# Optimization experiments

Measured on AMD Instinct MI355X. Metric: run time of the kernel, lower is better.

Reference implementation:

```python
import jax, jax.numpy as jnp
import numpy as np
from jax import lax

P = 2048
HIDDEN = 512
NUM_STEPS = 15
BATCH = 8192
SLOPE = 25.0  # snntorch surrogate.fast_sigmoid default slope


@jax.custom_vjp
def spike_fn(x):
    # Heaviside forward, fast-sigmoid surrogate backward.
    return (x > 0).astype(x.dtype)

def _spike_fwd(x):
    return spike_fn(x), x

def _spike_bwd(x, g):
    return (g / (SLOPE * jnp.abs(x) + 1.0) ** 2,)

spike_fn.defvjp(_spike_fwd, _spike_bwd)


def setup_inputs() -> dict:
    key = jax.random.key(0)
    ks = jax.random.split(key, 6)
    x = jax.random.randint(ks[0], (BATCH, 2), 0, P)
    embed = jax.random.normal(ks[1], (P, HIDDEN), dtype=jnp.float32)
    # Linear weights stored [in, out] (transpose of torch convention, same math)
    W1 = jax.random.normal(ks[2], (2 * HIDDEN, HIDDEN), dtype=jnp.float32) * (1.0 / np.sqrt(2 * HIDDEN))
    b1 = jnp.zeros((HIDDEN,), dtype=jnp.float32)
    W2 = jax.random.normal(ks[3], (HIDDEN, P), dtype=jnp.float32) * (1.0 / np.sqrt(HIDDEN))
    b2 = jnp.zeros((P,), dtype=jnp.float32)
    beta1 = jnp.float32(0.9)
    thr1 = jnp.float32(1.0)
    beta2 = jnp.float32(0.9)
    thr2 = jnp.float32(1.0)
    return {"x": x, "embed": embed, "W1": W1, "b1": b1, "W2": W2, "b2": b2,
            "beta1": beta1, "thr1": thr1, "beta2": beta2, "thr2": thr2}


def reference(x, embed, W1, b1, W2, b2, beta1, thr1, beta2, thr2):
    # clamp params as in the torch no-grad block (identity at init values)
    beta1 = jnp.clip(beta1, 0.1, 0.9)
    beta2 = jnp.clip(beta2, 0.1, 0.9)
    thr1 = jnp.clip(thr1, 0.1, None)
    thr2 = jnp.clip(thr2, 0.1, None)

    emb = embed[x].reshape(x.shape[0], -1)          # [B, 2*hidden]
    cur1 = emb @ W1 + b1                            # constant across steps

    mem1_0 = jnp.zeros((x.shape[0], HIDDEN), dtype=jnp.float32)
    mem2_0 = jnp.zeros((x.shape[0], P), dtype=jnp.float32)

    def step(carry, _):
        mem1, mem2 = carry
        # snntorch Leaky, reset_mechanism='subtract': reset from PREVIOUS mem, detached
        reset1 = lax.stop_gradient((mem1 - thr1 > 0).astype(mem1.dtype))
        mem1 = beta1 * mem1 + cur1 - reset1 * thr1
        spk1 = spike_fn(mem1 - thr1)
        cur2 = spk1 @ W2 + b2
        # lif2 has reset_mechanism='none'
        mem2 = beta2 * mem2 + cur2
        return (mem1, mem2), None

    (mem1, mem2), _ = lax.scan(step, (mem1_0, mem2_0), None, length=NUM_STEPS)
    return mem2  # output = last mem2
```

## Files before the change

### kernel.cpp

```cpp
#include <hip/hip_runtime.h>
#include <hip/hip_bf16.h>
#include <stdint.h>

typedef float    f32x4 __attribute__((ext_vector_type(4)));
typedef _Float16 f16x4 __attribute__((ext_vector_type(4)));
typedef _Float16 f16x8 __attribute__((ext_vector_type(8)));

#define NSTEPS 15

__global__ __launch_bounds__(256) void prep_kernel(
    const float* __restrict__ embed, const float* __restrict__ W1,
    const float* __restrict__ W2, const float* __restrict__ b2,
    const float* __restrict__ beta2p,
    _Float16* __restrict__ Ap, _Float16* __restrict__ Btp,
    _Float16* __restrict__ W2T, float* __restrict__ bias2s)
{
  __shared__ _Float16 sh[2][64][72];
  const int b = blockIdx.x;
  const int t = threadIdx.x;

  if (b < 1024) {
    const int i  = b * 256 + t;
    const int m  = i >> 7;
    const int k4 = (i & 127) * 4;
    f32x4 v = *(const f32x4*)&embed[(size_t)m * 512 + k4];
    f16x4 h0, h1;
#pragma unroll
    for (int j = 0; j < 4; ++j) {
      h0[j] = (_Float16)v[j];
      h1[j] = (_Float16)(v[j] - (float)h0[j]);
    }
    _Float16* r = Ap + (size_t)m * 1024 + k4;
    *(f16x4*)(r)       = h0;
    *(f16x4*)(r + 512) = h1;
  } else if (b < 1152) {
    const int idx = b - 1024;
    const int n0 = (idx & 7) * 64;
    const int k0 = ((idx >> 3) & 7) * 64;
    const int z  = idx >> 6;
    const int kk = t >> 4;
    const int n4 = (t & 15) * 4;
#pragma unroll
    for (int i = 0; i < 4; ++i) {
      f32x4 v = *(const f32x4*)&W1[(size_t)(z * 512 + k0 + kk + i * 16) * 512 + n0 + n4];
#pragma unroll
      for (int j = 0; j < 4; ++j) {
        float s = v[j] * 64.0f;
        _Float16 hi = (_Float16)s;
        sh[0][n4 + j][kk + i * 16] = hi;
        sh[1][n4 + j][kk + i * 16] = (_Float16)(s - (float)hi);
      }
    }
    __syncthreads();
#pragma unroll
    for (int i = 0; i < 2; ++i) {
      const int nn = (t >> 3) + i * 32;
      const int k8 = (t & 7) * 8;
      _Float16* r = Btp + (size_t)(z * 512 + n0 + nn) * 1024 + k0 + k8;
      *(uint4*)(r)       = *(const uint4*)&sh[0][nn][k8];
      *(uint4*)(r + 512) = *(const uint4*)&sh[1][nn][k8];
    }
  } else if (b < 1408) {
    const int idx = b - 1152;
    const int n0 = (idx & 31) * 64;
    const int k0 = (idx >> 5) * 64;
    const int kk = t >> 4;
    const int n4 = (t & 15) * 4;
#pragma unroll
    for (int i = 0; i < 4; ++i) {
      f32x4 v = *(const f32x4*)&W2[(size_t)(k0 + kk + i * 16) * 2048 + n0 + n4];
#pragma unroll
      for (int j = 0; j < 4; ++j) sh[0][n4 + j][kk + i * 16] = (_Float16)v[j];
    }
    __syncthreads();
#pragma unroll
    for (int i = 0; i < 2; ++i) {
      const int nn = (t >> 3) + i * 32;
      const int k8 = (t & 7) * 8;
      *(uint4*)&W2T[(size_t)(n0 + nn) * 512 + k0 + k8] = *(const uint4*)&sh[0][nn][k8];
    }
  } else {
    const float beta2 = fminf(fmaxf(beta2p[0], 0.1f), 0.9f);
    float cb = 0.0f;
    for (int i = 0; i < NSTEPS; ++i) cb = beta2 * cb + 1.0f;
    const int n = (b - 1408) * 256 + t;
    if (n < 2048) bias2s[n] = cb * b2[n];
  }
}

__device__ __forceinline__ void gld_lds16(const void* g, void* l) {
  __builtin_amdgcn_global_load_lds(
      (const __attribute__((address_space(1))) uint32_t*)g,
      (__attribute__((address_space(3))) uint32_t*)l, 16, 0, 0);
}

__global__ __launch_bounds__(256) void gemm1_kernel(
    const _Float16* __restrict__ Ap,
    const _Float16* __restrict__ Btp,
    float* __restrict__ Tp)
{
  __shared__ __align__(16) char lds[(128 + 64) * 128];
  char* AsB = lds;
  char* BsB = lds + 128 * 128;

  const int t    = threadIdx.x;
  const int lane = t & 63;
  const int wave = t >> 6;
  const int z    = blockIdx.y;

  int bid = blockIdx.x;
  bid = (bid & 7) * 32 + (bid >> 3);
  const int m0 = (bid >> 4) * 128;
  const int n0 = (bid & 15) * 64;

  f32x4 acc[2][4] = {};

  for (int kt = 0; kt < 12; ++kt) {
    const int k0   = z * 768 + kt * 64;
    const int acol = (k0 < 1024) ? k0 : k0 - 1024;
    const int bcol = (k0 < 1024) ? (k0 & 511) : k0 - 512;
#pragma unroll
    for (int i = 0; i < 4; ++i) {
      const int ob  = i * 4096 + wave * 1024;
      const int o   = ob + lane * 16;
      const int row = o >> 7;
      const int c   = ((o >> 4) & 7) ^ (row & 7);
      gld_lds16(Ap + ((size_t)(m0 + row) * 1024 + acol + c * 8), AsB + ob);
    }
#pragma unroll
    for (int i = 0; i < 2; ++i) {
      const int ob  = i * 4096 + wave * 1024;
      const int o   = ob + lane * 16;
      const int row = o >> 7;
      const int c   = ((o >> 4) & 7) ^ (row & 7);
      gld_lds16(Btp + ((size_t)(n0 + row) * 1024 + bcol + c * 8), BsB + ob);
    }
    asm volatile("s_waitcnt vmcnt(0)" ::: "memory");
    __syncthreads();

#pragma unroll
    for (int kk = 0; kk < 2; ++kk) {
      const int lc = (lane >> 4) + kk * 4;
      f16x8 af[2], bf[4];
#pragma unroll
      for (int mi = 0; mi < 2; ++mi) {
        const int row = wave * 32 + mi * 16 + (lane & 15);
        af[mi] = *(const f16x8*)(AsB + row * 128 + ((lc ^ (row & 7)) << 4));
      }
#pragma unroll
      for (int ni = 0; ni < 4; ++ni) {
        const int row = ni * 16 + (lane & 15);
        bf[ni] = *(const f16x8*)(BsB + row * 128 + ((lc ^ (row & 7)) << 4));
      }
#pragma unroll
      for (int mi = 0; mi < 2; ++mi)
#pragma unroll
        for (int ni = 0; ni < 4; ++ni)
          acc[mi][ni] = __builtin_amdgcn_mfma_f32_16x16x32_f16(
              af[mi], bf[ni], acc[mi][ni], 0, 0, 0);
    }
    __syncthreads();
  }

  float* Cz = Tp + (size_t)z * 2048 * 1024;
#pragma unroll
  for (int mi = 0; mi < 2; ++mi) {
    const int r0 = m0 + wave * 32 + mi * 16 + ((lane >> 4) << 2);
#pragma unroll
    for (int ni = 0; ni < 4; ++ni) {
      const int cc = n0 + ni * 16 + (lane & 15);
#pragma unroll
      for (int q = 0; q < 4; ++q)
        Cz[(size_t)(r0 + q) * 1024 + cc] = acc[mi][ni][q] * 0.015625f;
    }
  }
}

__global__ __launch_bounds__(256) void recur_kernel(
    const int* __restrict__ x,
    const float* __restrict__ Tp,
    const float* __restrict__ b1,
    const float* __restrict__ beta1p, const float* __restrict__ thr1p,
    const float* __restrict__ beta2p,
    _Float16* __restrict__ S)
{
  const float beta1 = fminf(fmaxf(beta1p[0], 0.1f), 0.9f);
  const float thr1  = fmaxf(thr1p[0], 0.1f);
  const float beta2 = fminf(fmaxf(beta2p[0], 0.1f), 0.9f);
  const size_t ZS = (size_t)2048 * 1024;

  const int t = threadIdx.x;
  const int b = blockIdx.x * 4 + (t >> 6);
  const int h = (t & 63) * 8;
  const int x0 = x[b * 2 + 0];
  const int x1 = x[b * 2 + 1];

  const float* p00 = &Tp[(size_t)x0 * 1024 + h];
  const float* p01 = &Tp[(size_t)x1 * 1024 + 512 + h];

  float cur[8];
#pragma unroll
  for (int half = 0; half < 2; ++half) {
    f32x4 a0 = *(const f32x4*)(p00 + half * 4);
    f32x4 a1 = *(const f32x4*)(p00 + ZS + half * 4);
    f32x4 c0 = *(const f32x4*)(p01 + half * 4);
    f32x4 c1 = *(const f32x4*)(p01 + ZS + half * 4);
    f32x4 e  = *(const f32x4*)&b1[h + half * 4];
#pragma unroll
    for (int j = 0; j < 4; ++j)
      cur[half * 4 + j] = (a0[j] + a1[j]) + (c0[j] + c1[j]) + e[j];
  }

  float m[8] = {}, s[8] = {};
#pragma unroll
  for (int st = 0; st < NSTEPS; ++st) {
#pragma unroll
    for (int j = 0; j < 8; ++j) {
      float r = (m[j] > thr1) ? thr1 : 0.0f;
      m[j] = beta1 * m[j] + cur[j] - r;
      float sp = (m[j] > thr1) ? 1.0f : 0.0f;
      s[j] = beta2 * s[j] + sp;
    }
  }

  __align__(16) _Float16 o[8];
#pragma unroll
  for (int j = 0; j < 8; ++j) o[j] = (_Float16)s[j];
  *(uint4*)&S[(size_t)b * 512 + h] = *(const uint4*)o;
}

__device__ __forceinline__ void g2_round(
    const _Float16* __restrict__ A, const _Float16* __restrict__ Bt,
    char* lds, int m0, int n0, int wave, int lane, int tile, int r)
{
  const int k0 = tile * 64;
  char* lb = lds + (tile % 3) * 49152;
  if (r < 4) {
    const int ob  = r * 8192 + wave * 1024;
    const int o   = ob + lane * 16;
    const int row = o >> 7;
    const int c   = ((o >> 4) & 7) ^ (row & 7);
    gld_lds16(A + ((size_t)(m0 + row) * 512 + k0 + c * 8), lb + ob);
  } else {
    const int ob  = (r - 4) * 8192 + wave * 1024;
    const int o   = ob + lane * 16;
    const int row = o >> 7;
    const int c   = ((o >> 4) & 7) ^ (row & 7);
    gld_lds16(Bt + ((size_t)(n0 + row) * 512 + k0 + c * 8), lb + 32768 + ob);
  }
}

template<int QA>
__device__ __forceinline__ void g2_mfma16(
    f32x4 (&acc)[8][2], const f16x8 (&af)[4][2], const f16x8 (&bf)[2][2])
{
#pragma unroll
  for (int kk = 0; kk < 2; ++kk)
#pragma unroll
    for (int mi = 0; mi < 4; ++mi)
#pragma unroll
      for (int ni = 0; ni < 2; ++ni)
        acc[QA * 4 + mi][ni] = __builtin_amdgcn_mfma_f32_16x16x32_f16(
            af[mi][kk], bf[ni][kk], acc[QA * 4 + mi][ni], 0, 0, 0);
}

template<int QA>
__device__ __forceinline__ void g2_lda(
    f16x8 (&af)[4][2], const char* lb, int wm, int lane)
{
#pragma unroll
  for (int mi = 0; mi < 4; ++mi) {
    const int row = wm * 128 + QA * 64 + mi * 16 + (lane & 15);
#pragma unroll
    for (int kk = 0; kk < 2; ++kk) {
      const int lc = (lane >> 4) + kk * 4;
      af[mi][kk] = *(const f16x8*)(lb + row * 128 + ((lc ^ (row & 7)) << 4));
    }
  }
}

__device__ __forceinline__ void g2_ldb(
    f16x8 (&bf)[2][2], const char* lb, int wn, int lane)
{
#pragma unroll
  for (int ni = 0; ni < 2; ++ni) {
    const int row = wn * 32 + ni * 16 + (lane & 15);
#pragma unroll
    for (int kk = 0; kk < 2; ++kk) {
      const int lc = (lane >> 4) + kk * 4;
      bf[ni][kk] = *(const f16x8*)(lb + 32768 + row * 128 + ((lc ^ (row & 7)) << 4));
    }
  }
}

__global__ __launch_bounds__(512, 2) void gemm2_pipe_kernel(
    const _Float16* __restrict__ A,
    const _Float16* __restrict__ Bt,
    const float* __restrict__ bias,
    float* __restrict__ C)
{
  __shared__ __align__(16) char lds[3 * 49152];

  const int t    = threadIdx.x;
  const int lane = t & 63;
  const int wave = t >> 6;
  const int wm   = wave >> 2;
  const int wn   = wave & 3;

  int bid = blockIdx.x;
  bid = (bid & 7) * 64 + (bid >> 3);
  const int m0 = (bid >> 4) * 256;
  const int n0 = (bid & 15) * 128;

  f32x4 acc[8][2] = {};
  f16x8 af[4][2], bf[2][2];

#pragma unroll
  for (int r = 0; r < 6; ++r) g2_round(A, Bt, lds, m0, n0, wave, lane, 0, r);
#pragma unroll
  for (int r = 0; r < 6; ++r) g2_round(A, Bt, lds, m0, n0, wave, lane, 1, r);
  asm volatile("s_waitcnt vmcnt(6)" ::: "memory");
  __builtin_amdgcn_s_barrier();

  for (int tt = 0; tt < 8; ++tt) {
    const char* lb = lds + (tt % 3) * 49152;
    const bool pf = (tt + 2 < 8);

    g2_lda<0>(af, lb, wm, lane);
    g2_ldb(bf, lb, wn, lane);
    if (pf) {
      g2_round(A, Bt, lds, m0, n0, wave, lane, tt + 2, 0);
      g2_round(A, Bt, lds, m0, n0, wave, lane, tt + 2, 1);
      g2_round(A, Bt, lds, m0, n0, wave, lane, tt + 2, 2);
    }
    __builtin_amdgcn_s_barrier();
    asm volatile("s_waitcnt lgkmcnt(0)" ::: "memory");
    __builtin_amdgcn_s_setprio(1);
    g2_mfma16<0>(acc, af, bf);
    __builtin_amdgcn_s_setprio(0);
    __builtin_amdgcn_s_barrier();

    g2_lda<1>(af, lb, wm, lane);
    if (pf) {
      g2_round(A, Bt, lds, m0, n0, wave, lane, tt + 2, 3);
      g2_round(A, Bt, lds, m0, n0, wave, lane, tt + 2, 4);
      g2_round(A, Bt, lds, m0, n0, wave, lane, tt + 2, 5);
    }
    __builtin_amdgcn_s_barrier();
    asm volatile("s_waitcnt lgkmcnt(0)" ::: "memory");
    __builtin_amdgcn_s_setprio(1);
    g2_mfma16<1>(acc, af, bf);
    __builtin_amdgcn_s_setprio(0);
    asm volatile("s_waitcnt vmcnt(6)" ::: "memory");
    __builtin_amdgcn_s_barrier();
  }

#pragma unroll
  for (int a = 0; a < 8; ++a) {
    const int r0 = m0 + wm * 128 + a * 16 + ((lane >> 4) << 2);
#pragma unroll
    for (int ni = 0; ni < 2; ++ni) {
      const int cc = n0 + wn * 32 + ni * 16 + (lane & 15);
      const float bv = bias[cc];
#pragma unroll
      for (int q = 0; q < 4; ++q)
        C[(size_t)(r0 + q) * 2048 + cc] = acc[a][ni][q] + bv;
    }
  }
}

extern "C" void kernel_launch(void* const* d_in, const int* in_sizes, int n_in,
                              void* d_out, int out_size, void* d_ws, size_t ws_size,
                              hipStream_t stream) {
  const int*   x     = (const int*)  d_in[0];
  const float* embed = (const float*)d_in[1];
  const float* W1    = (const float*)d_in[2];
  const float* b1    = (const float*)d_in[3];
  const float* W2    = (const float*)d_in[4];
  const float* b2    = (const float*)d_in[5];
  const float* beta1 = (const float*)d_in[6];
  const float* thr1  = (const float*)d_in[7];
  const float* beta2 = (const float*)d_in[8];
  float* out = (float*)d_out;

  char* ws = (char*)d_ws;
  float*    Tp     = (float*)   ws;
  _Float16* Ap     = (_Float16*)(ws + (16u << 20));
  _Float16* Btp    = (_Float16*)(ws + (20u << 20));
  _Float16* W2T    = (_Float16*)(ws + (22u << 20));
  _Float16* S      = (_Float16*)(ws + (24u << 20));
  float*    bias2s = (float*)   (ws + (32u << 20));

  prep_kernel<<<dim3(1416), 256, 0, stream>>>(embed, W1, W2, b2, beta2,
                                              Ap, Btp, W2T, bias2s);

  gemm1_kernel<<<dim3(256, 2), 256, 0, stream>>>(Ap, Btp, Tp);

  recur_kernel<<<dim3(2048), 256, 0, stream>>>(x, Tp, b1, beta1, thr1, beta2, S);

  gemm2_pipe_kernel<<<dim3(512), 512, 0, stream>>>(S, W2T, bias2s, out);
}
```

Measured before the change: 65.23 us.

## Replace split-K gemm1 partial outputs with in-block K reduction and 32x32 MFMA

```diff
diff --git a/kernel.cpp b/kernel.cpp
--- a/kernel.cpp
+++ b/kernel.cpp
@@ -2,18 +2,18 @@
 #include <hip/hip_bf16.h>
 #include <stdint.h>
 
-typedef float    f32x4 __attribute__((ext_vector_type(4)));
-typedef _Float16 f16x4 __attribute__((ext_vector_type(4)));
-typedef _Float16 f16x8 __attribute__((ext_vector_type(8)));
+typedef float    f32x4  __attribute__((ext_vector_type(4)));
+typedef float    f32x16 __attribute__((ext_vector_type(16)));
+typedef _Float16 f16x4  __attribute__((ext_vector_type(4)));
+typedef _Float16 f16x8  __attribute__((ext_vector_type(8)));
 
 #define NSTEPS 15
 
 __global__ __launch_bounds__(256) void prep_kernel(
     const float* __restrict__ embed, const float* __restrict__ W1,
-    const float* __restrict__ W2, const float* __restrict__ b2,
-    const float* __restrict__ beta2p,
+    const float* __restrict__ W2,
     _Float16* __restrict__ Ap, _Float16* __restrict__ Btp,
-    _Float16* __restrict__ W2T, float* __restrict__ bias2s)
+    _Float16* __restrict__ W2T)
 {
   __shared__ _Float16 sh[2][64][72];
   const int b = blockIdx.x;
@@ -60,7 +60,7 @@
       *(uint4*)(r)       = *(const uint4*)&sh[0][nn][k8];
       *(uint4*)(r + 512) = *(const uint4*)&sh[1][nn][k8];
     }
-  } else if (b < 1408) {
+  } else {
     const int idx = b - 1152;
     const int n0 = (idx & 31) * 64;
     const int k0 = (idx >> 5) * 64;
@@ -79,12 +79,6 @@
       const int k8 = (t & 7) * 8;
       *(uint4*)&W2T[(size_t)(n0 + nn) * 512 + k0 + k8] = *(const uint4*)&sh[0][nn][k8];
     }
-  } else {
-    const float beta2 = fminf(fmaxf(beta2p[0], 0.1f), 0.9f);
-    float cb = 0.0f;
-    for (int i = 0; i < NSTEPS; ++i) cb = beta2 * cb + 1.0f;
-    const int n = (b - 1408) * 256 + t;
-    if (n < 2048) bias2s[n] = cb * b2[n];
   }
 }
 
@@ -94,91 +88,111 @@
       (__attribute__((address_space(3))) uint32_t*)l, 16, 0, 0);
 }
 
-__global__ __launch_bounds__(256) void gemm1_kernel(
+__global__ __launch_bounds__(512) void gemm1_kernel(
     const _Float16* __restrict__ Ap,
     const _Float16* __restrict__ Btp,
-    float* __restrict__ Tp)
-{
-  __shared__ __align__(16) char lds[(128 + 64) * 128];
-  char* AsB = lds;
-  char* BsB = lds + 128 * 128;
+    float* __restrict__ T)
+{
+  __shared__ __align__(16) char lds[49152];
+  char* const ALDS = lds;
+  char* const BLDS = lds + 32768;
 
   const int t    = threadIdx.x;
   const int lane = t & 63;
   const int wave = t >> 6;
-  const int z    = blockIdx.y;
+  const int kh   = wave >> 2;
+  const int wq   = wave & 3;
+  const int wm   = wq >> 1;
+  const int wn   = wq & 1;
 
   int bid = blockIdx.x;
   bid = (bid & 7) * 32 + (bid >> 3);
   const int m0 = (bid >> 4) * 128;
   const int n0 = (bid & 15) * 64;
 
-  f32x4 acc[2][4] = {};
+  f32x16 acc[2] = {};
 
   for (int kt = 0; kt < 12; ++kt) {
-    const int k0   = z * 768 + kt * 64;
-    const int acol = (k0 < 1024) ? k0 : k0 - 1024;
-    const int bcol = (k0 < 1024) ? (k0 & 511) : k0 - 512;
-#pragma unroll
-    for (int i = 0; i < 4; ++i) {
-      const int ob  = i * 4096 + wave * 1024;
-      const int o   = ob + lane * 16;
-      const int row = o >> 7;
-      const int c   = ((o >> 4) & 7) ^ (row & 7);
-      gld_lds16(Ap + ((size_t)(m0 + row) * 1024 + acol + c * 8), AsB + ob);
-    }
-#pragma unroll
-    for (int i = 0; i < 2; ++i) {
-      const int ob  = i * 4096 + wave * 1024;
-      const int o   = ob + lane * 16;
-      const int row = o >> 7;
-      const int c   = ((o >> 4) & 7) ^ (row & 7);
-      gld_lds16(Btp + ((size_t)(n0 + row) * 1024 + bcol + c * 8), BsB + ob);
+#pragma unroll
+    for (int khs = 0; khs < 2; ++khs) {
+      const int vk0  = khs * 768 + kt * 64;
+      const int acol = (vk0 < 1024) ? vk0 : vk0 - 1024;
+      const int bcol = (vk0 < 1024) ? (vk0 & 511) : vk0 - 512;
+#pragma unroll
+      for (int i = 0; i < 2; ++i) {
+        const int ob  = (wave * 2 + i) * 1024;
+        const int o   = ob + lane * 16;
+        const int row = o >> 7;
+        const int c   = ((o >> 4) & 7) ^ (row & 7);
+        gld_lds16(Ap + ((size_t)(m0 + row) * 1024 + acol + c * 8),
+                  ALDS + khs * 16384 + ob);
+      }
+      {
+        const int ob  = wave * 1024;
+        const int o   = ob + lane * 16;
+        const int row = o >> 7;
+        const int c   = ((o >> 4) & 7) ^ (row & 7);
+        gld_lds16(Btp + ((size_t)(n0 + row) * 1024 + bcol + c * 8),
+                  BLDS + khs * 8192 + ob);
+      }
     }
     asm volatile("s_waitcnt vmcnt(0)" ::: "memory");
     __syncthreads();
 
-#pragma unroll
-    for (int kk = 0; kk < 2; ++kk) {
-      const int lc = (lane >> 4) + kk * 4;
-      f16x8 af[2], bf[4];
+    const char* Akh = ALDS + kh * 16384;
+    const char* Bkh = BLDS + kh * 8192;
+#pragma unroll
+    for (int kk = 0; kk < 4; ++kk) {
+      const int lc = kk * 2 + (lane >> 5);
+      f16x8 af[2], bf;
+      {
+        const int row = wn * 32 + (lane & 31);
+        bf = *(const f16x8*)(Bkh + row * 128 + ((lc ^ (row & 7)) << 4));
+      }
 #pragma unroll
       for (int mi = 0; mi < 2; ++mi) {
-        const int row = wave * 32 + mi * 16 + (lane & 15);
-        af[mi] = *(const f16x8*)(AsB + row * 128 + ((lc ^ (row & 7)) << 4));
-      }
-#pragma unroll
-      for (int ni = 0; ni < 4; ++ni) {
-        const int row = ni * 16 + (lane & 15);
-        bf[ni] = *(const f16x8*)(BsB + row * 128 + ((lc ^ (row & 7)) << 4));
+        const int row = wm * 64 + mi * 32 + (lane & 31);
+        af[mi] = *(const f16x8*)(Akh + row * 128 + ((lc ^ (row & 7)) << 4));
       }
 #pragma unroll
       for (int mi = 0; mi < 2; ++mi)
-#pragma unroll
-        for (int ni = 0; ni < 4; ++ni)
-          acc[mi][ni] = __builtin_amdgcn_mfma_f32_16x16x32_f16(
-              af[mi], bf[ni], acc[mi][ni], 0, 0, 0);
+        acc[mi] = __builtin_amdgcn_mfma_f32_32x32x16_f16(af[mi], bf, acc[mi], 0, 0, 0);
     }
     __syncthreads();
   }
 
-  float* Cz = Tp + (size_t)z * 2048 * 1024;
-#pragma unroll
-  for (int mi = 0; mi < 2; ++mi) {
-    const int r0 = m0 + wave * 32 + mi * 16 + ((lane >> 4) << 2);
-#pragma unroll
-    for (int ni = 0; ni < 4; ++ni) {
-      const int cc = n0 + ni * 16 + (lane & 15);
-#pragma unroll
-      for (int q = 0; q < 4; ++q)
-        Cz[(size_t)(r0 + q) * 1024 + cc] = acc[mi][ni][q] * 0.015625f;
+  if (kh == 1) {
+#pragma unroll
+    for (int mi = 0; mi < 2; ++mi)
+#pragma unroll
+      for (int rq = 0; rq < 4; ++rq) {
+        f32x4 v = { acc[mi][rq*4+0], acc[mi][rq*4+1], acc[mi][rq*4+2], acc[mi][rq*4+3] };
+        *(f32x4*)(lds + wq * 8192 + mi * 4096 + rq * 1024 + lane * 16) = v;
+      }
+  }
+  __syncthreads();
+  if (kh == 0) {
+    const int cc = n0 + wn * 32 + (lane & 31);
+#pragma unroll
+    for (int mi = 0; mi < 2; ++mi) {
+#pragma unroll
+      for (int rq = 0; rq < 4; ++rq) {
+        f32x4 v = *(const f32x4*)(lds + wq * 8192 + mi * 4096 + rq * 1024 + lane * 16);
+#pragma unroll
+        for (int j = 0; j < 4; ++j) acc[mi][rq*4+j] += v[j];
+      }
+#pragma unroll
+      for (int r = 0; r < 16; ++r) {
+        const int rr = m0 + wm * 64 + mi * 32 + (r & 3) + 8 * (r >> 2) + 4 * (lane >> 5);
+        T[(size_t)rr * 1024 + cc] = acc[mi][r] * 0.015625f;
+      }
     }
   }
 }
 
 __global__ __launch_bounds__(256) void recur_kernel(
     const int* __restrict__ x,
-    const float* __restrict__ Tp,
+    const float* __restrict__ T,
     const float* __restrict__ b1,
     const float* __restrict__ beta1p, const float* __restrict__ thr1p,
     const float* __restrict__ beta2p,
@@ -187,7 +201,6 @@
   const float beta1 = fminf(fmaxf(beta1p[0], 0.1f), 0.9f);
   const float thr1  = fmaxf(thr1p[0], 0.1f);
   const float beta2 = fminf(fmaxf(beta2p[0], 0.1f), 0.9f);
-  const size_t ZS = (size_t)2048 * 1024;
 
   const int t = threadIdx.x;
   const int b = blockIdx.x * 4 + (t >> 6);
@@ -195,20 +208,18 @@
   const int x0 = x[b * 2 + 0];
   const int x1 = x[b * 2 + 1];
 
-  const float* p00 = &Tp[(size_t)x0 * 1024 + h];
-  const float* p01 = &Tp[(size_t)x1 * 1024 + 512 + h];
+  const float* p0 = &T[(size_t)x0 * 1024 + h];
+  const float* p1 = &T[(size_t)x1 * 1024 + 512 + h];
 
   float cur[8];
 #pragma unroll
   for (int half = 0; half < 2; ++half) {
-    f32x4 a0 = *(const f32x4*)(p00 + half * 4);
-    f32x4 a1 = *(const f32x4*)(p00 + ZS + half * 4);
-    f32x4 c0 = *(const f32x4*)(p01 + half * 4);
-    f32x4 c1 = *(const f32x4*)(p01 + ZS + half * 4);
-    f32x4 e  = *(const f32x4*)&b1[h + half * 4];
+    f32x4 a = *(const f32x4*)(p0 + half * 4);
+    f32x4 c = *(const f32x4*)(p1 + half * 4);
+    f32x4 e = *(const f32x4*)&b1[h + half * 4];
 #pragma unroll
     for (int j = 0; j < 4; ++j)
-      cur[half * 4 + j] = (a0[j] + a1[j]) + (c0[j] + c1[j]) + e[j];
+      cur[half * 4 + j] = (a[j] + c[j]) + e[j];
   }
 
   float m[8] = {}, s[8] = {};
@@ -296,7 +307,8 @@
 __global__ __launch_bounds__(512, 2) void gemm2_pipe_kernel(
     const _Float16* __restrict__ A,
     const _Float16* __restrict__ Bt,
-    const float* __restrict__ bias,
+    const float* __restrict__ b2,
+    const float* __restrict__ beta2p,
     float* __restrict__ C)
 {
   __shared__ __align__(16) char lds[3 * 49152];
@@ -355,13 +367,17 @@
     __builtin_amdgcn_s_barrier();
   }
 
+  const float beta2 = fminf(fmaxf(beta2p[0], 0.1f), 0.9f);
+  float cb = 0.0f;
+  for (int i = 0; i < NSTEPS; ++i) cb = beta2 * cb + 1.0f;
+
 #pragma unroll
   for (int a = 0; a < 8; ++a) {
     const int r0 = m0 + wm * 128 + a * 16 + ((lane >> 4) << 2);
 #pragma unroll
     for (int ni = 0; ni < 2; ++ni) {
       const int cc = n0 + wn * 32 + ni * 16 + (lane & 15);
-      const float bv = bias[cc];
+      const float bv = cb * b2[cc];
 #pragma unroll
       for (int q = 0; q < 4; ++q)
         C[(size_t)(r0 + q) * 2048 + cc] = acc[a][ni][q] + bv;
@@ -384,19 +400,17 @@
   float* out = (float*)d_out;
 
   char* ws = (char*)d_ws;
-  float*    Tp     = (float*)   ws;
-  _Float16* Ap     = (_Float16*)(ws + (16u << 20));
-  _Float16* Btp    = (_Float16*)(ws + (20u << 20));
-  _Float16* W2T    = (_Float16*)(ws + (22u << 20));
-  _Float16* S      = (_Float16*)(ws + (24u << 20));
-  float*    bias2s = (float*)   (ws + (32u << 20));
-
-  prep_kernel<<<dim3(1416), 256, 0, stream>>>(embed, W1, W2, b2, beta2,
-                                              Ap, Btp, W2T, bias2s);
-
-  gemm1_kernel<<<dim3(256, 2), 256, 0, stream>>>(Ap, Btp, Tp);
-
-  recur_kernel<<<dim3(2048), 256, 0, stream>>>(x, Tp, b1, beta1, thr1, beta2, S);
-
-  gemm2_pipe_kernel<<<dim3(512), 512, 0, stream>>>(S, W2T, bias2s, out);
-}
+  float*    T      = (float*)   ws;
+  _Float16* Ap     = (_Float16*)(ws + ( 8u << 20));
+  _Float16* Btp    = (_Float16*)(ws + (12u << 20));
+  _Float16* W2T    = (_Float16*)(ws + (14u << 20));
+  _Float16* S      = (_Float16*)(ws + (16u << 20));
+
+  prep_kernel<<<dim3(1408), 256, 0, stream>>>(embed, W1, W2, Ap, Btp, W2T);
+
+  gemm1_kernel<<<dim3(256), 512, 0, stream>>>(Ap, Btp, T);
+
+  recur_kernel<<<dim3(2048), 256, 0, stream>>>(x, T, b1, beta1, thr1, beta2, S);
+
+  gemm2_pipe_kernel<<<dim3(512), 512, 0, stream>>>(S, W2T, b2, beta2, out);
+}
```

Result: slower. 68.59 us (+5.1%).

## Replace split-K gemm1 with smaller output tiles and fold bias scaling into gemm2

Applied to the files above, without the earlier changes.

```diff
diff --git a/kernel.cpp b/kernel.cpp
--- a/kernel.cpp
+++ b/kernel.cpp
@@ -10,10 +10,9 @@
 
 __global__ __launch_bounds__(256) void prep_kernel(
     const float* __restrict__ embed, const float* __restrict__ W1,
-    const float* __restrict__ W2, const float* __restrict__ b2,
-    const float* __restrict__ beta2p,
+    const float* __restrict__ W2,
     _Float16* __restrict__ Ap, _Float16* __restrict__ Btp,
-    _Float16* __restrict__ W2T, float* __restrict__ bias2s)
+    _Float16* __restrict__ W2T)
 {
   __shared__ _Float16 sh[2][64][72];
   const int b = blockIdx.x;
@@ -60,7 +59,7 @@
       *(uint4*)(r)       = *(const uint4*)&sh[0][nn][k8];
       *(uint4*)(r + 512) = *(const uint4*)&sh[1][nn][k8];
     }
-  } else if (b < 1408) {
+  } else {
     const int idx = b - 1152;
     const int n0 = (idx & 31) * 64;
     const int k0 = (idx >> 5) * 64;
@@ -79,12 +78,6 @@
       const int k8 = (t & 7) * 8;
       *(uint4*)&W2T[(size_t)(n0 + nn) * 512 + k0 + k8] = *(const uint4*)&sh[0][nn][k8];
     }
-  } else {
-    const float beta2 = fminf(fmaxf(beta2p[0], 0.1f), 0.9f);
-    float cb = 0.0f;
-    for (int i = 0; i < NSTEPS; ++i) cb = beta2 * cb + 1.0f;
-    const int n = (b - 1408) * 256 + t;
-    if (n < 2048) bias2s[n] = cb * b2[n];
   }
 }
 
@@ -97,31 +90,32 @@
 __global__ __launch_bounds__(256) void gemm1_kernel(
     const _Float16* __restrict__ Ap,
     const _Float16* __restrict__ Btp,
-    float* __restrict__ Tp)
-{
-  __shared__ __align__(16) char lds[(128 + 64) * 128];
+    float* __restrict__ T)
+{
+  __shared__ __align__(16) char lds[16384];
   char* AsB = lds;
-  char* BsB = lds + 128 * 128;
+  char* BsB = lds + 8192;
 
   const int t    = threadIdx.x;
   const int lane = t & 63;
   const int wave = t >> 6;
-  const int z    = blockIdx.y;
+  const int wm   = wave >> 1;
+  const int wn   = wave & 1;
 
   int bid = blockIdx.x;
-  bid = (bid & 7) * 32 + (bid >> 3);
-  const int m0 = (bid >> 4) * 128;
+  bid = (bid & 7) * 64 + (bid >> 3);
+  const int m0 = (bid >> 4) * 64;
   const int n0 = (bid & 15) * 64;
 
-  f32x4 acc[2][4] = {};
-
-  for (int kt = 0; kt < 12; ++kt) {
-    const int k0   = z * 768 + kt * 64;
-    const int acol = (k0 < 1024) ? k0 : k0 - 1024;
-    const int bcol = (k0 < 1024) ? (k0 & 511) : k0 - 512;
-#pragma unroll
-    for (int i = 0; i < 4; ++i) {
-      const int ob  = i * 4096 + wave * 1024;
+  f32x4 acc[2][2] = {};
+
+  for (int kt = 0; kt < 24; ++kt) {
+    const int vk0  = kt * 64;
+    const int acol = (vk0 < 1024) ? vk0 : vk0 - 1024;
+    const int bcol = (vk0 < 1024) ? (vk0 & 511) : vk0 - 512;
+#pragma unroll
+    for (int i = 0; i < 2; ++i) {
+      const int ob  = (wave * 2 + i) * 1024;
       const int o   = ob + lane * 16;
       const int row = o >> 7;
       const int c   = ((o >> 4) & 7) ^ (row & 7);
@@ -129,7 +123,7 @@
     }
 #pragma unroll
     for (int i = 0; i < 2; ++i) {
-      const int ob  = i * 4096 + wave * 1024;
+      const int ob  = (wave * 2 + i) * 1024;
       const int o   = ob + lane * 16;
       const int row = o >> 7;
       const int c   = ((o >> 4) & 7) ^ (row & 7);
@@ -141,44 +135,43 @@
 #pragma unroll
     for (int kk = 0; kk < 2; ++kk) {
       const int lc = (lane >> 4) + kk * 4;
-      f16x8 af[2], bf[4];
+      f16x8 af[2], bf[2];
 #pragma unroll
       for (int mi = 0; mi < 2; ++mi) {
-        const int row = wave * 32 + mi * 16 + (lane & 15);
+        const int row = wm * 32 + mi * 16 + (lane & 15);
         af[mi] = *(const f16x8*)(AsB + row * 128 + ((lc ^ (row & 7)) << 4));
       }
 #pragma unroll
-      for (int ni = 0; ni < 4; ++ni) {
-        const int row = ni * 16 + (lane & 15);
+      for (int ni = 0; ni < 2; ++ni) {
+        const int row = wn * 32 + ni * 16 + (lane & 15);
         bf[ni] = *(const f16x8*)(BsB + row * 128 + ((lc ^ (row & 7)) << 4));
       }
 #pragma unroll
       for (int mi = 0; mi < 2; ++mi)
 #pragma unroll
-        for (int ni = 0; ni < 4; ++ni)
+        for (int ni = 0; ni < 2; ++ni)
           acc[mi][ni] = __builtin_amdgcn_mfma_f32_16x16x32_f16(
               af[mi], bf[ni], acc[mi][ni], 0, 0, 0);
     }
     __syncthreads();
   }
 
-  float* Cz = Tp + (size_t)z * 2048 * 1024;
 #pragma unroll
   for (int mi = 0; mi < 2; ++mi) {
-    const int r0 = m0 + wave * 32 + mi * 16 + ((lane >> 4) << 2);
-#pragma unroll
-    for (int ni = 0; ni < 4; ++ni) {
-      const int cc = n0 + ni * 16 + (lane & 15);
+    const int r0 = m0 + wm * 32 + mi * 16 + ((lane >> 4) << 2);
+#pragma unroll
+    for (int ni = 0; ni < 2; ++ni) {
+      const int cc = n0 + wn * 32 + ni * 16 + (lane & 15);
 #pragma unroll
       for (int q = 0; q < 4; ++q)
-        Cz[(size_t)(r0 + q) * 1024 + cc] = acc[mi][ni][q] * 0.015625f;
+        T[(size_t)(r0 + q) * 1024 + cc] = acc[mi][ni][q] * 0.015625f;
     }
   }
 }
 
 __global__ __launch_bounds__(256) void recur_kernel(
     const int* __restrict__ x,
-    const float* __restrict__ Tp,
+    const float* __restrict__ T,
     const float* __restrict__ b1,
     const float* __restrict__ beta1p, const float* __restrict__ thr1p,
     const float* __restrict__ beta2p,
@@ -187,7 +180,6 @@
   const float beta1 = fminf(fmaxf(beta1p[0], 0.1f), 0.9f);
   const float thr1  = fmaxf(thr1p[0], 0.1f);
   const float beta2 = fminf(fmaxf(beta2p[0], 0.1f), 0.9f);
-  const size_t ZS = (size_t)2048 * 1024;
 
   const int t = threadIdx.x;
   const int b = blockIdx.x * 4 + (t >> 6);
@@ -195,20 +187,18 @@
   const int x0 = x[b * 2 + 0];
   const int x1 = x[b * 2 + 1];
 
-  const float* p00 = &Tp[(size_t)x0 * 1024 + h];
-  const float* p01 = &Tp[(size_t)x1 * 1024 + 512 + h];
+  const float* p0 = &T[(size_t)x0 * 1024 + h];
+  const float* p1 = &T[(size_t)x1 * 1024 + 512 + h];
 
   float cur[8];
 #pragma unroll
   for (int half = 0; half < 2; ++half) {
-    f32x4 a0 = *(const f32x4*)(p00 + half * 4);
-    f32x4 a1 = *(const f32x4*)(p00 + ZS + half * 4);
-    f32x4 c0 = *(const f32x4*)(p01 + half * 4);
-    f32x4 c1 = *(const f32x4*)(p01 + ZS + half * 4);
-    f32x4 e  = *(const f32x4*)&b1[h + half * 4];
+    f32x4 a = *(const f32x4*)(p0 + half * 4);
+    f32x4 c = *(const f32x4*)(p1 + half * 4);
+    f32x4 e = *(const f32x4*)&b1[h + half * 4];
 #pragma unroll
     for (int j = 0; j < 4; ++j)
-      cur[half * 4 + j] = (a0[j] + a1[j]) + (c0[j] + c1[j]) + e[j];
+      cur[half * 4 + j] = (a[j] + c[j]) + e[j];
   }
 
   float m[8] = {}, s[8] = {};
@@ -296,7 +286,8 @@
 __global__ __launch_bounds__(512, 2) void gemm2_pipe_kernel(
     const _Float16* __restrict__ A,
     const _Float16* __restrict__ Bt,
-    const float* __restrict__ bias,
+    const float* __restrict__ b2,
+    const float* __restrict__ beta2p,
     float* __restrict__ C)
 {
   __shared__ __align__(16) char lds[3 * 49152];
@@ -355,13 +346,17 @@
     __builtin_amdgcn_s_barrier();
   }
 
+  const float beta2 = fminf(fmaxf(beta2p[0], 0.1f), 0.9f);
+  float cb = 0.0f;
+  for (int i = 0; i < NSTEPS; ++i) cb = beta2 * cb + 1.0f;
+
 #pragma unroll
   for (int a = 0; a < 8; ++a) {
     const int r0 = m0 + wm * 128 + a * 16 + ((lane >> 4) << 2);
 #pragma unroll
     for (int ni = 0; ni < 2; ++ni) {
       const int cc = n0 + wn * 32 + ni * 16 + (lane & 15);
-      const float bv = bias[cc];
+      const float bv = cb * b2[cc];
 #pragma unroll
       for (int q = 0; q < 4; ++q)
         C[(size_t)(r0 + q) * 2048 + cc] = acc[a][ni][q] + bv;
@@ -384,19 +379,17 @@
   float* out = (float*)d_out;
 
   char* ws = (char*)d_ws;
-  float*    Tp     = (float*)   ws;
-  _Float16* Ap     = (_Float16*)(ws + (16u << 20));
-  _Float16* Btp    = (_Float16*)(ws + (20u << 20));
-  _Float16* W2T    = (_Float16*)(ws + (22u << 20));
-  _Float16* S      = (_Float16*)(ws + (24u << 20));
-  float*    bias2s = (float*)   (ws + (32u << 20));
-
-  prep_kernel<<<dim3(1416), 256, 0, stream>>>(embed, W1, W2, b2, beta2,
-                                              Ap, Btp, W2T, bias2s);
-
-  gemm1_kernel<<<dim3(256, 2), 256, 0, stream>>>(Ap, Btp, Tp);
-
-  recur_kernel<<<dim3(2048), 256, 0, stream>>>(x, Tp, b1, beta1, thr1, beta2, S);
-
-  gemm2_pipe_kernel<<<dim3(512), 512, 0, stream>>>(S, W2T, bias2s, out);
-}
+  float*    T   = (float*)   ws;
+  _Float16* Ap  = (_Float16*)(ws + ( 8u << 20));
+  _Float16* Btp = (_Float16*)(ws + (12u << 20));
+  _Float16* W2T = (_Float16*)(ws + (14u << 20));
+  _Float16* S   = (_Float16*)(ws + (16u << 20));
+
+  prep_kernel<<<dim3(1408), 256, 0, stream>>>(embed, W1, W2, Ap, Btp, W2T);
+
+  gemm1_kernel<<<dim3(512), 256, 0, stream>>>(Ap, Btp, T);
+
+  recur_kernel<<<dim3(2048), 256, 0, stream>>>(x, T, b1, beta1, thr1, beta2, S);
+
+  gemm2_pipe_kernel<<<dim3(512), 512, 0, stream>>>(S, W2T, b2, beta2, out);
+}
```

New measurement: 67.61 us. 1.04x slower.
